# Kernel tuning notes

Hardware: AMD Instinct MI355X
Metric: run time of the kernel (lower is better)

## Reference

```python
import jax, jax.numpy as jnp
import numpy as np

B, LQ, S, D, H = 8, 1024, 256, 1024, 16
HD = D // H
LN_EPS = 1e-5


def layer_norm(x, g, b):
    m = jnp.mean(x, axis=-1, keepdims=True)
    v = jnp.mean((x - m) ** 2, axis=-1, keepdims=True)
    return (x - m) / jnp.sqrt(v + LN_EPS) * g + b


def setup_inputs() -> dict:
    key = jax.random.key(0)
    ks = jax.random.split(key, 12)
    sc = 0.02
    p = lambda k, shp: jax.random.normal(k, shp, dtype=jnp.float32) * sc
    return {
        "memory": jax.random.normal(ks[0], (B, LQ, D // 2), dtype=jnp.float32),
        "gaze_features": jax.random.normal(ks[1], (B, LQ, D // 2), dtype=jnp.float32),
        "text_features": jax.random.normal(ks[2], (B, S, D), dtype=jnp.float32),
        "w_in": p(ks[3], (3 * D, D)),  # packed q,k,v in_proj (torch MHA layout)
        "b_in": jnp.zeros((3 * D,), jnp.float32),
        "w_o": p(ks[4], (D, D)),
        "b_o": jnp.zeros((D,), jnp.float32),
        "w1": p(ks[5], (D, D)),
        "b1": jnp.zeros((D,), jnp.float32),
        "w2": p(ks[6], (D, D)),
        "b2": jnp.zeros((D,), jnp.float32),
        "g1": jnp.ones((D,), jnp.float32),
        "be1": jnp.zeros((D,), jnp.float32),
        "g2": jnp.ones((D,), jnp.float32),
        "be2": jnp.zeros((D,), jnp.float32),
    }


def reference(memory, gaze_features, text_features, w_in, b_in, w_o, b_o,
              w1, b1, w2, b2, g1, be1, g2, be2):
    combined = jnp.concatenate([memory, gaze_features], axis=-1)  # [B, LQ, D]
    wq, wk, wv = w_in[:D], w_in[D:2 * D], w_in[2 * D:]
    bq, bk, bv = b_in[:D], b_in[D:2 * D], b_in[2 * D:]

    q = (combined @ wq.T + bq).reshape(B, LQ, H, HD)
    k = (text_features @ wk.T + bk).reshape(B, S, H, HD)
    v = (text_features @ wv.T + bv).reshape(B, S, H, HD)

    scores = jnp.einsum("bqhd,bkhd->bhqk", q, k) / jnp.sqrt(jnp.float32(HD))
    attn_w = jax.nn.softmax(scores, axis=-1)
    ctx = jnp.einsum("bhqk,bkhd->bqhd", attn_w, v).reshape(B, LQ, D)
    attn_output = ctx @ w_o.T + b_o  # [B, LQ, D]

    # dual FFN branches share linear1/linear2 (as in the source); dropout = eval identity
    ffn = jax.nn.relu(attn_output @ w1.T + b1) @ w2.T + b2
    refpoint_embed = layer_norm(ffn, g1, be1)
    tgt = layer_norm(ffn, g2, be2)

    # vectorized box decode (replaces the per-element Python loop)
    s = jax.nn.sigmoid(attn_output[..., :4])
    xc, yc, w, h = s[..., 0], s[..., 1], s[..., 2], s[..., 3]
    init_box_proposal = jnp.stack(
        [xc - w / 2, yc - h / 2, xc + w / 2, yc + h / 2], axis=-1)  # [B, LQ, 4]

    return refpoint_embed, tgt, init_box_proposal
```

## Files before the change

### kernel.cpp

```cpp
#include <hip/hip_runtime.h>


typedef unsigned short u16;
typedef unsigned int u32;
typedef __bf16 bf16x8 __attribute__((ext_vector_type(8)));
typedef float f32x4 __attribute__((ext_vector_type(4)));
typedef u16 u16x4 __attribute__((ext_vector_type(4)));

struct CvtArgs { const void* in[15]; };

__device__ __forceinline__ u16 f2bf(float f) {
  u32 u = __builtin_bit_cast(u32, f);
  u += 0x7fffu + ((u >> 16) & 1u);
  return (u16)(u >> 16);
}
__device__ __forceinline__ float bf2f(u16 h) {
  u32 u = ((u32)h) << 16;
  return __builtin_bit_cast(float, u);
}

struct WsPtrs {
  u16 *c_mem, *c_gaze, *c_text, *c_win, *c_bin, *c_wo, *c_bo, *c_w1, *c_b1,
      *c_w2, *c_b2, *c_g1, *c_be1, *c_g2, *c_be2;
  u16 *q, *k, *v, *ctx, *woT, *wf, *bfb, *h1;
  float* ffn;
};
__device__ __forceinline__ WsPtrs wsp(u16* C) {
  WsPtrs w;
  w.c_mem = C;                 w.c_gaze = C + 4194304;   w.c_text = C + 8388608;
  w.c_win = C + 10485760;      w.c_bin = C + 13631488;   w.c_wo = C + 13634560;
  w.c_bo = C + 14683136;       w.c_w1 = C + 14684160;    w.c_b1 = C + 15732736;
  w.c_w2 = C + 15733760;       w.c_b2 = C + 16782336;    w.c_g1 = C + 16783360;
  w.c_be1 = C + 16784384;      w.c_g2 = C + 16785408;    w.c_be2 = C + 16786432;
  u16* B2 = C + 16787488;
  w.q = B2;                    w.k = B2 + 8388608;       w.v = B2 + 10485760;
  w.ctx = B2 + 12582912;
  w.woT = B2 + 20971520;
  w.wf  = B2 + 22020096;
  w.bfb = B2 + 23068672;
  w.h1  = B2 + 29360128;
  w.ffn = (float*)B2;
  return w;
}

__device__ __forceinline__ void cvt_chunk(bool f32in, u16* dst,
                                          const void* const* srcs, u32 c8) {
  const u32 cum[16] = {0u, 4194304u, 8388608u, 10485760u, 13631488u, 13634560u,
                       14683136u, 14684160u, 15732736u, 15733760u, 16782336u,
                       16783360u, 16784384u, 16785408u, 16786432u, 16787456u};
  u32 base = c8 * 8u;
  int idx = 0;
#pragma unroll
  for (int i = 1; i < 15; ++i) if (base >= cum[i]) idx = i;
  u32 off = base - cum[idx];
  if (f32in) {
    const float* s = (const float*)srcs[idx] + off;
    float4 a = ((const float4*)s)[0];
    float4 b = ((const float4*)s)[1];
    u16 t[8] = {f2bf(a.x), f2bf(a.y), f2bf(a.z), f2bf(a.w),
                f2bf(b.x), f2bf(b.y), f2bf(b.z), f2bf(b.w)};
    *(uint4*)(dst + base) = *(const uint4*)t;
  } else {
    *(uint4*)(dst + base) = *(const uint4*)((const u16*)srcs[idx] + off);
  }
}

__global__ __launch_bounds__(256) void cvt_tr(CvtArgs a, u16* ws) {
  __shared__ u16 tile[128 * 136];
  const bool f32in = (((const u32*)a.in[11])[0] == 0x3F800000u);
  const int bid = blockIdx.x, tid = threadIdx.x;
  if (bid < 64) {
    WsPtrs w = wsp(ws);
    int tr = bid >> 3, tc = bid & 7;
#pragma unroll
    for (int p = 0; p < 8; ++p) {
      int t = p * 16 + (tid >> 4);
      int j8 = (tid & 15) * 8;
      u16 tmp[8];
      if (f32in) {
        const float* s = (const float*)a.in[5] + (size_t)(tr * 128 + t) * 1024 + tc * 128 + j8;
        float4 x = ((const float4*)s)[0], y = ((const float4*)s)[1];
        tmp[0]=f2bf(x.x); tmp[1]=f2bf(x.y); tmp[2]=f2bf(x.z); tmp[3]=f2bf(x.w);
        tmp[4]=f2bf(y.x); tmp[5]=f2bf(y.y); tmp[6]=f2bf(y.z); tmp[7]=f2bf(y.w);
      } else {
        *(uint4*)tmp = *(const uint4*)((const u16*)a.in[5] + (size_t)(tr * 128 + t) * 1024 + tc * 128 + j8);
      }
      *(uint4*)&tile[t * 136 + j8] = *(const uint4*)tmp;
    }
    __syncthreads();
#pragma unroll
    for (int p = 0; p < 8; ++p) {
      int j = p * 16 + (tid >> 4);
      int t8 = (tid & 15) * 8;
      u16 tmp[8];
#pragma unroll
      for (int i = 0; i < 8; ++i) tmp[i] = tile[(t8 + i) * 136 + j];
      *(uint4*)(w.woT + (size_t)(tc * 128 + j) * 1024 + tr * 128 + t8) = *(const uint4*)tmp;
    }
  } else {
    u32 c8 = (u32)(bid - 64) * 256u + tid;
    if (c8 < 2098432u) cvt_chunk(f32in, ws, a.in, c8);
  }
}

__device__ __forceinline__ void gemm_core(
    u16* sA, u16* sB,
    const u16* A0, const u16* A1, int Ksplit, int lda0, int lda1,
    const u16* W, const u16* bias, void* out, int N, int K,
    int mode, int lg, int m0, int n0)
{
  const int tid = threadIdx.x;
  const int wave = tid >> 6, lane = tid & 63;
  const int quad = lane >> 4, l16 = lane & 15;
  const int wm = wave >> 1, wn = wave & 1;

  f32x4 acc[4][4];
#pragma unroll
  for (int i = 0; i < 4; ++i)
#pragma unroll
    for (int j = 0; j < 4; ++j) acc[i][j] = (f32x4){0.f, 0.f, 0.f, 0.f};

  for (int k0 = 0; k0 < K; k0 += 128) {
#pragma unroll
    for (int qi = 0; qi < 8; ++qi) {
      int p = (wave * 8 + qi) * 64 + lane;
      int row = p >> 4;
      int c = (p & 15) ^ (row & 7);
      int gk = k0 + (c << 3);
      const u16* srcA = (gk < Ksplit) ? (A0 + (size_t)(m0 + row) * lda0 + gk)
                                      : (A1 + (size_t)(m0 + row) * lda1 + (gk - Ksplit));
      __builtin_amdgcn_global_load_lds(
          (const __attribute__((address_space(1))) void*)srcA,
          (__attribute__((address_space(3))) void*)&sA[(size_t)(wave * 8 + qi) * 512],
          16, 0, 0);
      const u16* srcB = W + (size_t)(n0 + row) * K + gk;
      __builtin_amdgcn_global_load_lds(
          (const __attribute__((address_space(1))) void*)srcB,
          (__attribute__((address_space(3))) void*)&sB[(size_t)(wave * 8 + qi) * 512],
          16, 0, 0);
    }
    __syncthreads();
#pragma unroll
    for (int ks = 0; ks < 4; ++ks) {
      const int ch = (ks << 2) + quad;
      bf16x8 af[4], bw[4];
#pragma unroll
      for (int i = 0; i < 4; ++i) {
        int row = wm * 64 + i * 16 + l16;
        af[i] = *(const bf16x8*)&sA[(row << 7) + ((ch ^ (row & 7)) << 3)];
      }
#pragma unroll
      for (int j = 0; j < 4; ++j) {
        int row = wn * 64 + j * 16 + l16;
        bw[j] = *(const bf16x8*)&sB[(row << 7) + ((ch ^ (row & 7)) << 3)];
      }
#pragma unroll
      for (int i = 0; i < 4; ++i)
#pragma unroll
        for (int j = 0; j < 4; ++j)
          acc[i][j] = __builtin_amdgcn_mfma_f32_16x16x32_bf16(af[i], bw[j], acc[i][j], 0, 0, 0);
    }
    __syncthreads();
  }

#pragma unroll
  for (int i = 0; i < 4; ++i) {
#pragma unroll
    for (int j = 0; j < 4; ++j) {
      int n = n0 + wn * 64 + j * 16 + l16;
      float bv = bias ? bf2f(bias[n]) : 0.f;
#pragma unroll
      for (int rr = 0; rr < 4; ++rr) {
        int m = m0 + wm * 64 + i * 16 + quad * 4 + rr;
        float val = acc[i][j][rr] + bv;
        if (mode == 1) val = fmaxf(val, 0.f);
        if (mode == 2) {
          ((float*)out)[(size_t)m * N + n] = val;
        } else if (mode <= 1) {
          ((u16*)out)[(size_t)m * N + n] = f2bf(val);
        } else if (mode == 3) {
          int b = m >> lg, l = m & ((1 << lg) - 1);
          int h = n >> 6, d = n & 63;
          ((u16*)out)[((size_t)((b * 16 + h)) << (lg + 6)) + (l << 6) + d] = f2bf(val);
        } else {
          int b = m >> lg, s = m & ((1 << lg) - 1);
          int h = n >> 6, d = n & 63;
          ((u16*)out)[((size_t)(((b * 16 + h) << 6) + d) << lg) + s] = f2bf(val);
        }
      }
    }
  }
}

__global__ __launch_bounds__(256) void qkvwf(u16* ws) {
  __shared__ u16 lds[32768];
  WsPtrs w = wsp(ws);
  const int bid = blockIdx.x, tid = threadIdx.x;
  if (bid < 4) {
    int i = bid * 256 + tid;
    const u16* w1row = w.c_w1 + (size_t)i * 1024;
    float acc = bf2f(w.c_b1[i]);
    for (int kk = 0; kk < 1024; kk += 8) {
      bf16x8 wv = *(const bf16x8*)(w1row + kk);
      bf16x8 bv = *(const bf16x8*)(w.c_bo + kk);
#pragma unroll
      for (int j = 0; j < 8; ++j) acc += (float)wv[j] * (float)bv[j];
    }
    w.bfb[i] = f2bf(acc);
  } else if (bid < 68) {
    int u = bid - 4;
    gemm_core(lds, lds + 16384, w.c_w1, w.c_w1, 1024, 1024, 1024,
              w.woT, nullptr, w.wf, 1024, 1024, 0, 0,
              (u >> 3) * 128, (u & 7) * 128);
  } else if (bid < 580) {
    int u = bid - 68;
    gemm_core(lds, lds + 16384, w.c_mem, w.c_gaze, 512, 512, 512,
              w.c_win, w.c_bin, w.q, 1024, 1024, 3, 10,
              (u >> 3) * 128, (u & 7) * 128);
  } else if (bid < 708) {
    int u = bid - 580;
    gemm_core(lds, lds + 16384, w.c_text, w.c_text, 1024, 1024, 1024,
              w.c_win + 1048576, w.c_bin + 1024, w.k, 1024, 1024, 3, 8,
              (u >> 3) * 128, (u & 7) * 128);
  } else {
    int u = bid - 708;
    gemm_core(lds, lds + 16384, w.c_text, w.c_text, 1024, 1024, 1024,
              w.c_win + 2097152, w.c_bin + 2048, w.v, 1024, 1024, 4, 8,
              (u >> 3) * 128, (u & 7) * 128);
  }
}

__global__ __launch_bounds__(256) void attn_kernel(u16* ws) {
  __shared__ u16 sV[64 * 256];
  __shared__ u16 sKP[256 * 64];
  WsPtrs w = wsp(ws);
  const int tid = threadIdx.x;
  const int wave = tid >> 6, lane = tid & 63;
  const int quad = lane >> 4, l16 = lane & 15;
  const int qb = blockIdx.x & 15, bh = blockIdx.x >> 4;

  {
    int rr = tid >> 3, c8 = (tid & 7) << 3;
    const u16* kb = w.k + (size_t)bh * 16384;
#pragma unroll
    for (int p = 0; p < 8; ++p) {
      int row = p * 32 + rr;
      uint4 val = *(const uint4*)(kb + row * 64 + c8);
      *(uint4*)&sKP[(row << 6) + ((((c8 >> 3) ^ (row & 7))) << 3)] = val;
    }
    int r2 = tid >> 5, c8b = (tid & 31) << 3;
    const u16* vb = w.v + (size_t)bh * 16384;
#pragma unroll
    for (int p = 0; p < 8; ++p) {
      int row = p * 8 + r2;
      uint4 val = *(const uint4*)(vb + (row << 8) + c8b);
      *(uint4*)&sV[(row << 8) + ((((c8b >> 3) ^ (row & 7))) << 3)] = val;
    }
  }
  bf16x8 aq[2];
  {
    const u16* qrow = w.q + ((size_t)bh * 1024 + qb * 64 + wave * 16 + l16) * 64 + quad * 8;
    aq[0] = *(const bf16x8*)(qrow);
    aq[1] = *(const bf16x8*)(qrow + 32);
  }
  __syncthreads();

  f32x4 sc[16];
#pragma unroll
  for (int nt = 0; nt < 16; ++nt) sc[nt] = (f32x4){0.f, 0.f, 0.f, 0.f};
#pragma unroll
  for (int ks = 0; ks < 2; ++ks) {
    const int ch = (ks << 2) + quad;
#pragma unroll
    for (int nt = 0; nt < 16; ++nt) {
      int row = nt * 16 + l16;
      bf16x8 bk = *(const bf16x8*)&sKP[(row << 6) + ((ch ^ (row & 7)) << 3)];
      sc[nt] = __builtin_amdgcn_mfma_f32_16x16x32_bf16(aq[ks], bk, sc[nt], 0, 0, 0);
    }
  }
#pragma unroll
  for (int rr = 0; rr < 4; ++rr) {
    float mx = -1e30f;
#pragma unroll
    for (int nt = 0; nt < 16; ++nt) mx = fmaxf(mx, sc[nt][rr]);
    for (int off = 1; off < 16; off <<= 1) mx = fmaxf(mx, __shfl_xor(mx, off, 64));
    float sum = 0.f;
#pragma unroll
    for (int nt = 0; nt < 16; ++nt) {
      float p = __expf((sc[nt][rr] - mx) * 0.125f);
      sc[nt][rr] = p; sum += p;
    }
    for (int off = 1; off < 16; off <<= 1) sum += __shfl_xor(sum, off, 64);
    float inv = 1.f / sum;
#pragma unroll
    for (int nt = 0; nt < 16; ++nt) sc[nt][rr] *= inv;
  }
  __syncthreads();
#pragma unroll
  for (int nt = 0; nt < 16; ++nt)
#pragma unroll
    for (int rr = 0; rr < 4; ++rr) {
      int row = wave * 16 + quad * 4 + rr;
      int col = nt * 16 + l16;
      sKP[(row << 8) + (((col >> 3) ^ (row & 7)) << 3) + (col & 7)] = f2bf(sc[nt][rr]);
    }
  __syncthreads();

  f32x4 o[4];
#pragma unroll
  for (int j = 0; j < 4; ++j) o[j] = (f32x4){0.f, 0.f, 0.f, 0.f};
#pragma unroll
  for (int ks = 0; ks < 8; ++ks) {
    const int ch = (ks << 2) + quad;
    int prow = wave * 16 + l16;
    bf16x8 ap = *(const bf16x8*)&sKP[(prow << 8) + ((ch ^ (prow & 7)) << 3)];
#pragma unroll
    for (int j = 0; j < 4; ++j) {
      int vrow = j * 16 + l16;
      bf16x8 bv = *(const bf16x8*)&sV[(vrow << 8) + ((ch ^ (vrow & 7)) << 3)];
      o[j] = __builtin_amdgcn_mfma_f32_16x16x32_bf16(ap, bv, o[j], 0, 0, 0);
    }
  }
  const int b = bh >> 4, h = bh & 15;
#pragma unroll
  for (int j = 0; j < 4; ++j)
#pragma unroll
    for (int rr = 0; rr < 4; ++rr) {
      int m = qb * 64 + wave * 16 + quad * 4 + rr;
      int d = h * 64 + j * 16 + l16;
      w.ctx[((size_t)b * 1024 + m) * 1024 + d] = f2bf(o[j][rr]);
    }
}

__global__ __launch_bounds__(256) void h1box(u16* ws, void* out, const void* g1orig) {
  __shared__ u16 lds[32768];
  WsPtrs w = wsp(ws);
  const int bid = blockIdx.x, tid = threadIdx.x;
  if (bid < 32) {
    const bool f32out = (((const u32*)g1orig)[0] == 0x3F800000u);
    int m = bid * 256 + tid;
    const u16* crow = w.ctx + (size_t)m * 1024;
    float a0 = bf2f(w.c_bo[0]), a1 = bf2f(w.c_bo[1]);
    float a2 = bf2f(w.c_bo[2]), a3 = bf2f(w.c_bo[3]);
    for (int kk = 0; kk < 1024; kk += 8) {
      bf16x8 cv = *(const bf16x8*)(crow + kk);
      bf16x8 w0 = *(const bf16x8*)(w.c_wo + kk);
      bf16x8 w1 = *(const bf16x8*)(w.c_wo + 1024 + kk);
      bf16x8 w2 = *(const bf16x8*)(w.c_wo + 2048 + kk);
      bf16x8 w3 = *(const bf16x8*)(w.c_wo + 3072 + kk);
#pragma unroll
      for (int j = 0; j < 8; ++j) {
        float c = (float)cv[j];
        a0 += c * (float)w0[j]; a1 += c * (float)w1[j];
        a2 += c * (float)w2[j]; a3 += c * (float)w3[j];
      }
    }
    float s0 = 1.f / (1.f + __expf(-a0)), s1 = 1.f / (1.f + __expf(-a1));
    float s2 = 1.f / (1.f + __expf(-a2)), s3 = 1.f / (1.f + __expf(-a3));
    float o0 = s0 - s2 * 0.5f, o1 = s1 - s3 * 0.5f;
    float o2 = s0 + s2 * 0.5f, o3 = s1 + s3 * 0.5f;
    if (f32out) {
      float* fo = (float*)out + 16777216;
      *(float4*)(fo + (size_t)m * 4) = make_float4(o0, o1, o2, o3);
    } else {
      u16* bo = (u16*)out + 16777216;
      u16x4 o; o[0] = f2bf(o0); o[1] = f2bf(o1); o[2] = f2bf(o2); o[3] = f2bf(o3);
      *(u16x4*)(bo + (size_t)m * 4) = o;
    }
  } else {
    int u = bid - 32;
    gemm_core(lds, lds + 16384, w.ctx, w.ctx, 1024, 1024, 1024,
              w.wf, w.bfb, w.h1, 1024, 1024, 1, 0,
              (u >> 3) * 128, (u & 7) * 128);
  }
}

__global__ __launch_bounds__(256) void w2gemm(u16* ws) {
  __shared__ u16 lds[32768];
  WsPtrs w = wsp(ws);
  gemm_core(lds, lds + 16384, w.h1, w.h1, 1024, 1024, 1024,
            w.c_w2, w.c_b2, w.ffn, 1024, 1024, 2, 0,
            (blockIdx.x >> 3) * 128, (blockIdx.x & 7) * 128);
}

__global__ __launch_bounds__(256) void ln_kernel(u16* ws, void* outv, const void* g1orig) {
  WsPtrs w = wsp(ws);
  const bool f32out = (((const u32*)g1orig)[0] == 0x3F800000u);
  const int row = blockIdx.x, tid = threadIdx.x;
  const float4 x4 = ((const float4*)(w.ffn + (size_t)row * 1024))[tid];
  float s = x4.x + x4.y + x4.z + x4.w;
  float s2 = x4.x * x4.x + x4.y * x4.y + x4.z * x4.z + x4.w * x4.w;
  for (int m = 32; m >= 1; m >>= 1) { s += __shfl_xor(s, m, 64); s2 += __shfl_xor(s2, m, 64); }
  __shared__ float red[8];
  int wv = tid >> 6;
  if ((tid & 63) == 0) { red[wv] = s; red[4 + wv] = s2; }
  __syncthreads();
  s = red[0] + red[1] + red[2] + red[3];
  s2 = red[4] + red[5] + red[6] + red[7];
  float mean = s * (1.f / 1024.f);
  float var = s2 * (1.f / 1024.f) - mean * mean;
  float inv = rsqrtf(var + 1e-5f);
  int c = tid * 4;
  float y[4] = {(x4.x - mean) * inv, (x4.y - mean) * inv, (x4.z - mean) * inv, (x4.w - mean) * inv};
  float v1[4], v2[4];
#pragma unroll
  for (int i = 0; i < 4; ++i) {
    v1[i] = y[i] * bf2f(w.c_g1[c + i]) + bf2f(w.c_be1[c + i]);
    v2[i] = y[i] * bf2f(w.c_g2[c + i]) + bf2f(w.c_be2[c + i]);
  }
  if (f32out) {
    float* fo = (float*)outv;
    *(float4*)(fo + (size_t)row * 1024 + c) = make_float4(v1[0], v1[1], v1[2], v1[3]);
    *(float4*)(fo + 8388608 + (size_t)row * 1024 + c) = make_float4(v2[0], v2[1], v2[2], v2[3]);
  } else {
    u16* out = (u16*)outv;
    u16x4 o1, o2;
#pragma unroll
    for (int i = 0; i < 4; ++i) { o1[i] = f2bf(v1[i]); o2[i] = f2bf(v2[i]); }
    *(u16x4*)(out + (size_t)row * 1024 + c) = o1;
    *(u16x4*)(out + 8388608 + (size_t)row * 1024 + c) = o2;
  }
}

extern "C" void kernel_launch(void* const* d_in, const int* in_sizes, int n_in,
                              void* d_out, int out_size, void* d_ws, size_t ws_size,
                              hipStream_t stream) {
  CvtArgs ca;
  for (int i = 0; i < 15; ++i) ca.in[i] = d_in[i];
  u16* ws = (u16*)d_ws;
  dim3 blk(256);
  cvt_tr<<<dim3(8261), blk, 0, stream>>>(ca, ws);
  qkvwf<<<dim3(836), blk, 0, stream>>>(ws);
  attn_kernel<<<dim3(2048), blk, 0, stream>>>(ws);
  h1box<<<dim3(544), blk, 0, stream>>>(ws, d_out, d_in[11]);
  w2gemm<<<dim3(512), blk, 0, stream>>>(ws);
  ln_kernel<<<dim3(8192), blk, 0, stream>>>(ws, d_out, d_in[11]);
}
```

Baseline: 313.6 us.

## Fuse box decode, FFN GEMMs and layernorm into one persistent kernel with atomic counters

Merges the box/h1 kernel, the W2 GEMM and the layernorm kernel into a single 512-block kernel. Cross-block dependencies are handled with global atomic row-tile counters and ticket-based work assignment, and the counters are reset at the start of the attention kernel. The FFN intermediate is now stored in bf16 instead of fp32, and the box decode is split across 16 lanes per row. It also reorders the blocks in qkvwf so the big Q GEMM is scheduled first. The goal is to remove launch gaps and the fp32 round trip, at the cost of spin-wait synchronisation that depends on all blocks being co-resident, plus reduced precision for the LN input.

```diff
diff --git a/kernel.cpp b/kernel.cpp
--- a/kernel.cpp
+++ b/kernel.cpp
@@ -18,12 +18,19 @@
   u32 u = ((u32)h) << 16;
   return __builtin_bit_cast(float, u);
 }
-
+__device__ __forceinline__ u32 aadd(u32* p) {
+  return __hip_atomic_fetch_add(p, 1u, __ATOMIC_RELAXED, __HIP_MEMORY_SCOPE_AGENT);
+}
+__device__ __forceinline__ u32 aload(const u32* p) {
+  return __hip_atomic_load(p, __ATOMIC_RELAXED, __HIP_MEMORY_SCOPE_AGENT);
+}
+
+#define B2OFF 16787488
+#define SYNC_U32 ((B2OFF + 23069696) / 2)
 struct WsPtrs {
   u16 *c_mem, *c_gaze, *c_text, *c_win, *c_bin, *c_wo, *c_bo, *c_w1, *c_b1,
       *c_w2, *c_b2, *c_g1, *c_be1, *c_g2, *c_be2;
-  u16 *q, *k, *v, *ctx, *woT, *wf, *bfb, *h1;
-  float* ffn;
+  u16 *q, *k, *v, *ctx, *woT, *wf, *bfb, *h1, *ffnb;
 };
 __device__ __forceinline__ WsPtrs wsp(u16* C) {
   WsPtrs w;
@@ -32,14 +39,14 @@
   w.c_bo = C + 14683136;       w.c_w1 = C + 14684160;    w.c_b1 = C + 15732736;
   w.c_w2 = C + 15733760;       w.c_b2 = C + 16782336;    w.c_g1 = C + 16783360;
   w.c_be1 = C + 16784384;      w.c_g2 = C + 16785408;    w.c_be2 = C + 16786432;
-  u16* B2 = C + 16787488;
+  u16* B2 = C + B2OFF;
   w.q = B2;                    w.k = B2 + 8388608;       w.v = B2 + 10485760;
   w.ctx = B2 + 12582912;
   w.woT = B2 + 20971520;
   w.wf  = B2 + 22020096;
   w.bfb = B2 + 23068672;
   w.h1  = B2 + 29360128;
-  w.ffn = (float*)B2;
+  w.ffnb = B2;
   return w;
 }
 
@@ -174,9 +181,7 @@
         int m = m0 + wm * 64 + i * 16 + quad * 4 + rr;
         float val = acc[i][j][rr] + bv;
         if (mode == 1) val = fmaxf(val, 0.f);
-        if (mode == 2) {
-          ((float*)out)[(size_t)m * N + n] = val;
-        } else if (mode <= 1) {
+        if (mode <= 1) {
           ((u16*)out)[(size_t)m * N + n] = f2bf(val);
         } else if (mode == 3) {
           int b = m >> lg, l = m & ((1 << lg) - 1);
@@ -196,8 +201,27 @@
   __shared__ u16 lds[32768];
   WsPtrs w = wsp(ws);
   const int bid = blockIdx.x, tid = threadIdx.x;
-  if (bid < 4) {
-    int i = bid * 256 + tid;
+  if (bid < 512) {
+    gemm_core(lds, lds + 16384, w.c_mem, w.c_gaze, 512, 512, 512,
+              w.c_win, w.c_bin, w.q, 1024, 1024, 3, 10,
+              (bid >> 3) * 128, (bid & 7) * 128);
+  } else if (bid < 640) {
+    int u = bid - 512;
+    gemm_core(lds, lds + 16384, w.c_text, w.c_text, 1024, 1024, 1024,
+              w.c_win + 1048576, w.c_bin + 1024, w.k, 1024, 1024, 3, 8,
+              (u >> 3) * 128, (u & 7) * 128);
+  } else if (bid < 768) {
+    int u = bid - 640;
+    gemm_core(lds, lds + 16384, w.c_text, w.c_text, 1024, 1024, 1024,
+              w.c_win + 2097152, w.c_bin + 2048, w.v, 1024, 1024, 4, 8,
+              (u >> 3) * 128, (u & 7) * 128);
+  } else if (bid < 832) {
+    int u = bid - 768;
+    gemm_core(lds, lds + 16384, w.c_w1, w.c_w1, 1024, 1024, 1024,
+              w.woT, nullptr, w.wf, 1024, 1024, 0, 0,
+              (u >> 3) * 128, (u & 7) * 128);
+  } else {
+    int i = (bid - 832) * 256 + tid;
     const u16* w1row = w.c_w1 + (size_t)i * 1024;
     float acc = bf2f(w.c_b1[i]);
     for (int kk = 0; kk < 1024; kk += 8) {
@@ -207,26 +231,6 @@
       for (int j = 0; j < 8; ++j) acc += (float)wv[j] * (float)bv[j];
     }
     w.bfb[i] = f2bf(acc);
-  } else if (bid < 68) {
-    int u = bid - 4;
-    gemm_core(lds, lds + 16384, w.c_w1, w.c_w1, 1024, 1024, 1024,
-              w.woT, nullptr, w.wf, 1024, 1024, 0, 0,
-              (u >> 3) * 128, (u & 7) * 128);
-  } else if (bid < 580) {
-    int u = bid - 68;
-    gemm_core(lds, lds + 16384, w.c_mem, w.c_gaze, 512, 512, 512,
-              w.c_win, w.c_bin, w.q, 1024, 1024, 3, 10,
-              (u >> 3) * 128, (u & 7) * 128);
-  } else if (bid < 708) {
-    int u = bid - 580;
-    gemm_core(lds, lds + 16384, w.c_text, w.c_text, 1024, 1024, 1024,
-              w.c_win + 1048576, w.c_bin + 1024, w.k, 1024, 1024, 3, 8,
-              (u >> 3) * 128, (u & 7) * 128);
-  } else {
-    int u = bid - 708;
-    gemm_core(lds, lds + 16384, w.c_text, w.c_text, 1024, 1024, 1024,
-              w.c_win + 2097152, w.c_bin + 2048, w.v, 1024, 1024, 4, 8,
-              (u >> 3) * 128, (u & 7) * 128);
   }
 }
 
@@ -235,6 +239,7 @@
   __shared__ u16 sKP[256 * 64];
   WsPtrs w = wsp(ws);
   const int tid = threadIdx.x;
+  if (blockIdx.x == 0 && tid < 130) ((u32*)ws)[SYNC_U32 + tid] = 0;
   const int wave = tid >> 6, lane = tid & 63;
   const int quad = lane >> 4, l16 = lane & 15;
   const int qb = blockIdx.x & 15, bh = blockIdx.x >> 4;
@@ -332,22 +337,30 @@
     }
 }
 
-__global__ __launch_bounds__(256) void h1box(u16* ws, void* out, const void* g1orig) {
+__global__ __launch_bounds__(256, 2) void ffn_mega(u16* ws, void* out, const void* g1orig) {
   __shared__ u16 lds[32768];
+  __shared__ u32 s_t;
   WsPtrs w = wsp(ws);
-  const int bid = blockIdx.x, tid = threadIdx.x;
-  if (bid < 32) {
-    const bool f32out = (((const u32*)g1orig)[0] == 0x3F800000u);
-    int m = bid * 256 + tid;
-    const u16* crow = w.ctx + (size_t)m * 1024;
-    float a0 = bf2f(w.c_bo[0]), a1 = bf2f(w.c_bo[1]);
-    float a2 = bf2f(w.c_bo[2]), a3 = bf2f(w.c_bo[3]);
-    for (int kk = 0; kk < 1024; kk += 8) {
+  u32* cnt1 = (u32*)ws + SYNC_U32;
+  u32* cnt2 = cnt1 + 64;
+  u32* tick1 = cnt1 + 128;
+  u32* tick2 = cnt1 + 129;
+  const bool f32out = (((const u32*)g1orig)[0] == 0x3F800000u);
+  const int u = blockIdx.x, tid = threadIdx.x;
+  const int r16 = tid >> 4, l4 = tid & 15;
+
+  {
+    int m = u * 16 + r16;
+    int k0 = l4 * 64;
+    const u16* crow = w.ctx + (size_t)m * 1024 + k0;
+    float a0 = 0.f, a1 = 0.f, a2 = 0.f, a3 = 0.f;
+#pragma unroll
+    for (int kk = 0; kk < 64; kk += 8) {
       bf16x8 cv = *(const bf16x8*)(crow + kk);
-      bf16x8 w0 = *(const bf16x8*)(w.c_wo + kk);
-      bf16x8 w1 = *(const bf16x8*)(w.c_wo + 1024 + kk);
-      bf16x8 w2 = *(const bf16x8*)(w.c_wo + 2048 + kk);
-      bf16x8 w3 = *(const bf16x8*)(w.c_wo + 3072 + kk);
+      bf16x8 w0 = *(const bf16x8*)(w.c_wo + k0 + kk);
+      bf16x8 w1 = *(const bf16x8*)(w.c_wo + 1024 + k0 + kk);
+      bf16x8 w2 = *(const bf16x8*)(w.c_wo + 2048 + k0 + kk);
+      bf16x8 w3 = *(const bf16x8*)(w.c_wo + 3072 + k0 + kk);
 #pragma unroll
       for (int j = 0; j < 8; ++j) {
         float c = (float)cv[j];
@@ -355,70 +368,116 @@
         a2 += c * (float)w2[j]; a3 += c * (float)w3[j];
       }
     }
-    float s0 = 1.f / (1.f + __expf(-a0)), s1 = 1.f / (1.f + __expf(-a1));
-    float s2 = 1.f / (1.f + __expf(-a2)), s3 = 1.f / (1.f + __expf(-a3));
-    float o0 = s0 - s2 * 0.5f, o1 = s1 - s3 * 0.5f;
-    float o2 = s0 + s2 * 0.5f, o3 = s1 + s3 * 0.5f;
-    if (f32out) {
-      float* fo = (float*)out + 16777216;
-      *(float4*)(fo + (size_t)m * 4) = make_float4(o0, o1, o2, o3);
-    } else {
-      u16* bo = (u16*)out + 16777216;
-      u16x4 o; o[0] = f2bf(o0); o[1] = f2bf(o1); o[2] = f2bf(o2); o[3] = f2bf(o3);
-      *(u16x4*)(bo + (size_t)m * 4) = o;
-    }
-  } else {
-    int u = bid - 32;
-    gemm_core(lds, lds + 16384, w.ctx, w.ctx, 1024, 1024, 1024,
-              w.wf, w.bfb, w.h1, 1024, 1024, 1, 0,
-              (u >> 3) * 128, (u & 7) * 128);
-  }
-}
-
-__global__ __launch_bounds__(256) void w2gemm(u16* ws) {
-  __shared__ u16 lds[32768];
-  WsPtrs w = wsp(ws);
-  gemm_core(lds, lds + 16384, w.h1, w.h1, 1024, 1024, 1024,
-            w.c_w2, w.c_b2, w.ffn, 1024, 1024, 2, 0,
-            (blockIdx.x >> 3) * 128, (blockIdx.x & 7) * 128);
-}
-
-__global__ __launch_bounds__(256) void ln_kernel(u16* ws, void* outv, const void* g1orig) {
-  WsPtrs w = wsp(ws);
-  const bool f32out = (((const u32*)g1orig)[0] == 0x3F800000u);
-  const int row = blockIdx.x, tid = threadIdx.x;
-  const float4 x4 = ((const float4*)(w.ffn + (size_t)row * 1024))[tid];
-  float s = x4.x + x4.y + x4.z + x4.w;
-  float s2 = x4.x * x4.x + x4.y * x4.y + x4.z * x4.z + x4.w * x4.w;
-  for (int m = 32; m >= 1; m >>= 1) { s += __shfl_xor(s, m, 64); s2 += __shfl_xor(s2, m, 64); }
-  __shared__ float red[8];
-  int wv = tid >> 6;
-  if ((tid & 63) == 0) { red[wv] = s; red[4 + wv] = s2; }
-  __syncthreads();
-  s = red[0] + red[1] + red[2] + red[3];
-  s2 = red[4] + red[5] + red[6] + red[7];
-  float mean = s * (1.f / 1024.f);
-  float var = s2 * (1.f / 1024.f) - mean * mean;
-  float inv = rsqrtf(var + 1e-5f);
-  int c = tid * 4;
-  float y[4] = {(x4.x - mean) * inv, (x4.y - mean) * inv, (x4.z - mean) * inv, (x4.w - mean) * inv};
-  float v1[4], v2[4];
-#pragma unroll
-  for (int i = 0; i < 4; ++i) {
-    v1[i] = y[i] * bf2f(w.c_g1[c + i]) + bf2f(w.c_be1[c + i]);
-    v2[i] = y[i] * bf2f(w.c_g2[c + i]) + bf2f(w.c_be2[c + i]);
-  }
-  if (f32out) {
-    float* fo = (float*)outv;
-    *(float4*)(fo + (size_t)row * 1024 + c) = make_float4(v1[0], v1[1], v1[2], v1[3]);
-    *(float4*)(fo + 8388608 + (size_t)row * 1024 + c) = make_float4(v2[0], v2[1], v2[2], v2[3]);
-  } else {
-    u16* out = (u16*)outv;
-    u16x4 o1, o2;
-#pragma unroll
-    for (int i = 0; i < 4; ++i) { o1[i] = f2bf(v1[i]); o2[i] = f2bf(v2[i]); }
-    *(u16x4*)(out + (size_t)row * 1024 + c) = o1;
-    *(u16x4*)(out + 8388608 + (size_t)row * 1024 + c) = o2;
+    for (int off = 1; off < 16; off <<= 1) {
+      a0 += __shfl_xor(a0, off, 64); a1 += __shfl_xor(a1, off, 64);
+      a2 += __shfl_xor(a2, off, 64); a3 += __shfl_xor(a3, off, 64);
+    }
+    if (l4 == 0) {
+      a0 += bf2f(w.c_bo[0]); a1 += bf2f(w.c_bo[1]);
+      a2 += bf2f(w.c_bo[2]); a3 += bf2f(w.c_bo[3]);
+      float s0 = 1.f / (1.f + __expf(-a0)), s1 = 1.f / (1.f + __expf(-a1));
+      float s2 = 1.f / (1.f + __expf(-a2)), s3 = 1.f / (1.f + __expf(-a3));
+      float o0 = s0 - s2 * 0.5f, o1 = s1 - s3 * 0.5f;
+      float o2 = s0 + s2 * 0.5f, o3 = s1 + s3 * 0.5f;
+      if (f32out) {
+        float* fo = (float*)out + 16777216;
+        *(float4*)(fo + (size_t)m * 4) = make_float4(o0, o1, o2, o3);
+      } else {
+        u16* bo = (u16*)out + 16777216;
+        u16x4 o; o[0] = f2bf(o0); o[1] = f2bf(o1); o[2] = f2bf(o2); o[3] = f2bf(o3);
+        *(u16x4*)(bo + (size_t)m * 4) = o;
+      }
+    }
+  }
+
+  gemm_core(lds, lds + 16384, w.ctx, w.ctx, 1024, 1024, 1024,
+            w.wf, w.bfb, w.h1, 1024, 1024, 1, 0, (u >> 3) * 128, (u & 7) * 128);
+  __syncthreads();
+  if (tid == 0) { __threadfence(); aadd(&cnt1[u >> 3]); }
+
+  if (tid == 0) s_t = aadd(tick1);
+  __syncthreads();
+  {
+    u32 t = s_t;
+    int ms2 = t >> 3;
+    if (tid == 0) {
+      while (aload(&cnt1[ms2]) < 8u) __builtin_amdgcn_s_sleep(16);
+      __threadfence();
+    }
+    __syncthreads();
+    gemm_core(lds, lds + 16384, w.h1, w.h1, 1024, 1024, 1024,
+              w.c_w2, w.c_b2, w.ffnb, 1024, 1024, 0, 0, ms2 * 128, (t & 7) * 128);
+    __syncthreads();
+    if (tid == 0) { __threadfence(); aadd(&cnt2[ms2]); }
+  }
+
+  if (tid == 0) s_t = aadd(tick2);
+  __syncthreads();
+  {
+    u32 t2 = s_t;
+    if (t2 < 64u) {
+      if (tid == 0) {
+        while (aload(&cnt2[t2]) < 8u) __builtin_amdgcn_s_sleep(16);
+        __threadfence();
+      }
+      __syncthreads();
+#pragma unroll
+      for (int rr = 0; rr < 8; ++rr) {
+        int row = (int)t2 * 128 + rr * 16 + r16;
+        int c0 = l4 * 64;
+        const u16* fr = w.ffnb + (size_t)row * 1024 + c0;
+        float s = 0.f, s2 = 0.f;
+#pragma unroll
+        for (int kk = 0; kk < 64; kk += 8) {
+          bf16x8 xv = *(const bf16x8*)(fr + kk);
+#pragma unroll
+          for (int j = 0; j < 8; ++j) { float x = (float)xv[j]; s += x; s2 += x * x; }
+        }
+        for (int off = 1; off < 16; off <<= 1) {
+          s += __shfl_xor(s, off, 64); s2 += __shfl_xor(s2, off, 64);
+        }
+        float mean = s * (1.f / 1024.f);
+        float var = s2 * (1.f / 1024.f) - mean * mean;
+        float inv = rsqrtf(var + 1e-5f);
+        if (f32out) {
+          float* fo = (float*)out;
+#pragma unroll
+          for (int kk = 0; kk < 64; kk += 8) {
+            bf16x8 xv = *(const bf16x8*)(fr + kk);
+            float t1v[8], t2v[8];
+#pragma unroll
+            for (int j = 0; j < 8; ++j) {
+              float y = ((float)xv[j] - mean) * inv;
+              int c = c0 + kk + j;
+              t1v[j] = y * bf2f(w.c_g1[c]) + bf2f(w.c_be1[c]);
+              t2v[j] = y * bf2f(w.c_g2[c]) + bf2f(w.c_be2[c]);
+            }
+            size_t o1 = (size_t)row * 1024 + c0 + kk;
+            *(float4*)(fo + o1) = make_float4(t1v[0], t1v[1], t1v[2], t1v[3]);
+            *(float4*)(fo + o1 + 4) = make_float4(t1v[4], t1v[5], t1v[6], t1v[7]);
+            *(float4*)(fo + 8388608 + o1) = make_float4(t2v[0], t2v[1], t2v[2], t2v[3]);
+            *(float4*)(fo + 8388608 + o1 + 4) = make_float4(t2v[4], t2v[5], t2v[6], t2v[7]);
+          }
+        } else {
+          u16* uo = (u16*)out;
+#pragma unroll
+          for (int kk = 0; kk < 64; kk += 8) {
+            bf16x8 xv = *(const bf16x8*)(fr + kk);
+            u16 t1v[8], t2v[8];
+#pragma unroll
+            for (int j = 0; j < 8; ++j) {
+              float y = ((float)xv[j] - mean) * inv;
+              int c = c0 + kk + j;
+              t1v[j] = f2bf(y * bf2f(w.c_g1[c]) + bf2f(w.c_be1[c]));
+              t2v[j] = f2bf(y * bf2f(w.c_g2[c]) + bf2f(w.c_be2[c]));
+            }
+            size_t o1 = (size_t)row * 1024 + c0 + kk;
+            *(uint4*)(uo + o1) = *(const uint4*)t1v;
+            *(uint4*)(uo + 8388608 + o1) = *(const uint4*)t2v;
+          }
+        }
+      }
+    }
   }
 }
 
@@ -432,7 +491,5 @@
   cvt_tr<<<dim3(8261), blk, 0, stream>>>(ca, ws);
   qkvwf<<<dim3(836), blk, 0, stream>>>(ws);
   attn_kernel<<<dim3(2048), blk, 0, stream>>>(ws);
-  h1box<<<dim3(544), blk, 0, stream>>>(ws, d_out, d_in[11]);
-  w2gemm<<<dim3(512), blk, 0, stream>>>(ws);
-  ln_kernel<<<dim3(8192), blk, 0, stream>>>(ws, d_out, d_in[11]);
-}
+  ffn_mega<<<dim3(512), blk, 0, stream>>>(ws, d_out, d_in[11]);
+}
```

Measured after the change: 527.6 us. 1.68x slower.

## Store FFN output in bf16, spread box decode across GEMM blocks, reorder qkvwf blocks

Applied to the files above, without the earlier changes.

The FFN output written by the second GEMM is stored as bf16 instead of fp32, which halves the traffic between that GEMM and the layer-norm kernel. The box-decode dot products used to run in 32 serial tail blocks. They are now split across all 512 h1 GEMM blocks, with 16 lanes per row and a shuffle reduction before each block does its GEMM tile. The qkvwf block ordering is also changed so the large Q/K/V GEMM tiles are scheduled first and the small bias dot-product blocks come last. The cost is lower precision on the FFN intermediate before layer norm.

```diff
diff --git a/kernel.cpp b/kernel.cpp
--- a/kernel.cpp
+++ b/kernel.cpp
@@ -22,8 +22,7 @@
 struct WsPtrs {
   u16 *c_mem, *c_gaze, *c_text, *c_win, *c_bin, *c_wo, *c_bo, *c_w1, *c_b1,
       *c_w2, *c_b2, *c_g1, *c_be1, *c_g2, *c_be2;
-  u16 *q, *k, *v, *ctx, *woT, *wf, *bfb, *h1;
-  float* ffn;
+  u16 *q, *k, *v, *ctx, *woT, *wf, *bfb, *h1, *ffnb;
 };
 __device__ __forceinline__ WsPtrs wsp(u16* C) {
   WsPtrs w;
@@ -39,7 +38,7 @@
   w.wf  = B2 + 22020096;
   w.bfb = B2 + 23068672;
   w.h1  = B2 + 29360128;
-  w.ffn = (float*)B2;
+  w.ffnb = B2;
   return w;
 }
 
@@ -174,9 +173,7 @@
         int m = m0 + wm * 64 + i * 16 + quad * 4 + rr;
         float val = acc[i][j][rr] + bv;
         if (mode == 1) val = fmaxf(val, 0.f);
-        if (mode == 2) {
-          ((float*)out)[(size_t)m * N + n] = val;
-        } else if (mode <= 1) {
+        if (mode <= 1) {
           ((u16*)out)[(size_t)m * N + n] = f2bf(val);
         } else if (mode == 3) {
           int b = m >> lg, l = m & ((1 << lg) - 1);
@@ -196,8 +193,27 @@
   __shared__ u16 lds[32768];
   WsPtrs w = wsp(ws);
   const int bid = blockIdx.x, tid = threadIdx.x;
-  if (bid < 4) {
-    int i = bid * 256 + tid;
+  if (bid < 512) {
+    gemm_core(lds, lds + 16384, w.c_mem, w.c_gaze, 512, 512, 512,
+              w.c_win, w.c_bin, w.q, 1024, 1024, 3, 10,
+              (bid >> 3) * 128, (bid & 7) * 128);
+  } else if (bid < 640) {
+    int u = bid - 512;
+    gemm_core(lds, lds + 16384, w.c_text, w.c_text, 1024, 1024, 1024,
+              w.c_win + 1048576, w.c_bin + 1024, w.k, 1024, 1024, 3, 8,
+              (u >> 3) * 128, (u & 7) * 128);
+  } else if (bid < 768) {
+    int u = bid - 640;
+    gemm_core(lds, lds + 16384, w.c_text, w.c_text, 1024, 1024, 1024,
+              w.c_win + 2097152, w.c_bin + 2048, w.v, 1024, 1024, 4, 8,
+              (u >> 3) * 128, (u & 7) * 128);
+  } else if (bid < 832) {
+    int u = bid - 768;
+    gemm_core(lds, lds + 16384, w.c_w1, w.c_w1, 1024, 1024, 1024,
+              w.woT, nullptr, w.wf, 1024, 1024, 0, 0,
+              (u >> 3) * 128, (u & 7) * 128);
+  } else {
+    int i = (bid - 832) * 256 + tid;
     const u16* w1row = w.c_w1 + (size_t)i * 1024;
     float acc = bf2f(w.c_b1[i]);
     for (int kk = 0; kk < 1024; kk += 8) {
@@ -207,26 +223,6 @@
       for (int j = 0; j < 8; ++j) acc += (float)wv[j] * (float)bv[j];
     }
     w.bfb[i] = f2bf(acc);
-  } else if (bid < 68) {
-    int u = bid - 4;
-    gemm_core(lds, lds + 16384, w.c_w1, w.c_w1, 1024, 1024, 1024,
-              w.woT, nullptr, w.wf, 1024, 1024, 0, 0,
-              (u >> 3) * 128, (u & 7) * 128);
-  } else if (bid < 580) {
-    int u = bid - 68;
-    gemm_core(lds, lds + 16384, w.c_mem, w.c_gaze, 512, 512, 512,
-              w.c_win, w.c_bin, w.q, 1024, 1024, 3, 10,
-              (u >> 3) * 128, (u & 7) * 128);
-  } else if (bid < 708) {
-    int u = bid - 580;
-    gemm_core(lds, lds + 16384, w.c_text, w.c_text, 1024, 1024, 1024,
-              w.c_win + 1048576, w.c_bin + 1024, w.k, 1024, 1024, 3, 8,
-              (u >> 3) * 128, (u & 7) * 128);
-  } else {
-    int u = bid - 708;
-    gemm_core(lds, lds + 16384, w.c_text, w.c_text, 1024, 1024, 1024,
-              w.c_win + 2097152, w.c_bin + 2048, w.v, 1024, 1024, 4, 8,
-              (u >> 3) * 128, (u & 7) * 128);
   }
 }
 
@@ -335,19 +331,21 @@
 __global__ __launch_bounds__(256) void h1box(u16* ws, void* out, const void* g1orig) {
   __shared__ u16 lds[32768];
   WsPtrs w = wsp(ws);
-  const int bid = blockIdx.x, tid = threadIdx.x;
-  if (bid < 32) {
+  const int u = blockIdx.x, tid = threadIdx.x;
+  const int r16 = tid >> 4, l4 = tid & 15;
+  {
     const bool f32out = (((const u32*)g1orig)[0] == 0x3F800000u);
-    int m = bid * 256 + tid;
-    const u16* crow = w.ctx + (size_t)m * 1024;
-    float a0 = bf2f(w.c_bo[0]), a1 = bf2f(w.c_bo[1]);
-    float a2 = bf2f(w.c_bo[2]), a3 = bf2f(w.c_bo[3]);
-    for (int kk = 0; kk < 1024; kk += 8) {
+    int m = u * 16 + r16;
+    int k0 = l4 * 64;
+    const u16* crow = w.ctx + (size_t)m * 1024 + k0;
+    float a0 = 0.f, a1 = 0.f, a2 = 0.f, a3 = 0.f;
+#pragma unroll
+    for (int kk = 0; kk < 64; kk += 8) {
       bf16x8 cv = *(const bf16x8*)(crow + kk);
-      bf16x8 w0 = *(const bf16x8*)(w.c_wo + kk);
-      bf16x8 w1 = *(const bf16x8*)(w.c_wo + 1024 + kk);
-      bf16x8 w2 = *(const bf16x8*)(w.c_wo + 2048 + kk);
-      bf16x8 w3 = *(const bf16x8*)(w.c_wo + 3072 + kk);
+      bf16x8 w0 = *(const bf16x8*)(w.c_wo + k0 + kk);
+      bf16x8 w1 = *(const bf16x8*)(w.c_wo + 1024 + k0 + kk);
+      bf16x8 w2 = *(const bf16x8*)(w.c_wo + 2048 + k0 + kk);
+      bf16x8 w3 = *(const bf16x8*)(w.c_wo + 3072 + k0 + kk);
 #pragma unroll
       for (int j = 0; j < 8; ++j) {
         float c = (float)cv[j];
@@ -355,31 +353,36 @@
         a2 += c * (float)w2[j]; a3 += c * (float)w3[j];
       }
     }
-    float s0 = 1.f / (1.f + __expf(-a0)), s1 = 1.f / (1.f + __expf(-a1));
-    float s2 = 1.f / (1.f + __expf(-a2)), s3 = 1.f / (1.f + __expf(-a3));
-    float o0 = s0 - s2 * 0.5f, o1 = s1 - s3 * 0.5f;
-    float o2 = s0 + s2 * 0.5f, o3 = s1 + s3 * 0.5f;
-    if (f32out) {
-      float* fo = (float*)out + 16777216;
-      *(float4*)(fo + (size_t)m * 4) = make_float4(o0, o1, o2, o3);
-    } else {
-      u16* bo = (u16*)out + 16777216;
-      u16x4 o; o[0] = f2bf(o0); o[1] = f2bf(o1); o[2] = f2bf(o2); o[3] = f2bf(o3);
-      *(u16x4*)(bo + (size_t)m * 4) = o;
-    }
-  } else {
-    int u = bid - 32;
-    gemm_core(lds, lds + 16384, w.ctx, w.ctx, 1024, 1024, 1024,
-              w.wf, w.bfb, w.h1, 1024, 1024, 1, 0,
-              (u >> 3) * 128, (u & 7) * 128);
-  }
+    for (int off = 1; off < 16; off <<= 1) {
+      a0 += __shfl_xor(a0, off, 64); a1 += __shfl_xor(a1, off, 64);
+      a2 += __shfl_xor(a2, off, 64); a3 += __shfl_xor(a3, off, 64);
+    }
+    if (l4 == 0) {
+      a0 += bf2f(w.c_bo[0]); a1 += bf2f(w.c_bo[1]);
+      a2 += bf2f(w.c_bo[2]); a3 += bf2f(w.c_bo[3]);
+      float s0 = 1.f / (1.f + __expf(-a0)), s1 = 1.f / (1.f + __expf(-a1));
+      float s2 = 1.f / (1.f + __expf(-a2)), s3 = 1.f / (1.f + __expf(-a3));
+      float o0 = s0 - s2 * 0.5f, o1 = s1 - s3 * 0.5f;
+      float o2 = s0 + s2 * 0.5f, o3 = s1 + s3 * 0.5f;
+      if (f32out) {
+        float* fo = (float*)out + 16777216;
+        *(float4*)(fo + (size_t)m * 4) = make_float4(o0, o1, o2, o3);
+      } else {
+        u16* bo = (u16*)out + 16777216;
+        u16x4 o; o[0] = f2bf(o0); o[1] = f2bf(o1); o[2] = f2bf(o2); o[3] = f2bf(o3);
+        *(u16x4*)(bo + (size_t)m * 4) = o;
+      }
+    }
+  }
+  gemm_core(lds, lds + 16384, w.ctx, w.ctx, 1024, 1024, 1024,
+            w.wf, w.bfb, w.h1, 1024, 1024, 1, 0, (u >> 3) * 128, (u & 7) * 128);
 }
 
 __global__ __launch_bounds__(256) void w2gemm(u16* ws) {
   __shared__ u16 lds[32768];
   WsPtrs w = wsp(ws);
   gemm_core(lds, lds + 16384, w.h1, w.h1, 1024, 1024, 1024,
-            w.c_w2, w.c_b2, w.ffn, 1024, 1024, 2, 0,
+            w.c_w2, w.c_b2, w.ffnb, 1024, 1024, 0, 0,
             (blockIdx.x >> 3) * 128, (blockIdx.x & 7) * 128);
 }
 
@@ -387,9 +390,11 @@
   WsPtrs w = wsp(ws);
   const bool f32out = (((const u32*)g1orig)[0] == 0x3F800000u);
   const int row = blockIdx.x, tid = threadIdx.x;
-  const float4 x4 = ((const float4*)(w.ffn + (size_t)row * 1024))[tid];
-  float s = x4.x + x4.y + x4.z + x4.w;
-  float s2 = x4.x * x4.x + x4.y * x4.y + x4.z * x4.z + x4.w * x4.w;
+  int c = tid * 4;
+  u16x4 xr = *(const u16x4*)(w.ffnb + (size_t)row * 1024 + c);
+  float x[4] = {bf2f(xr[0]), bf2f(xr[1]), bf2f(xr[2]), bf2f(xr[3])};
+  float s = x[0] + x[1] + x[2] + x[3];
+  float s2 = x[0]*x[0] + x[1]*x[1] + x[2]*x[2] + x[3]*x[3];
   for (int m = 32; m >= 1; m >>= 1) { s += __shfl_xor(s, m, 64); s2 += __shfl_xor(s2, m, 64); }
   __shared__ float red[8];
   int wv = tid >> 6;
@@ -400,8 +405,7 @@
   float mean = s * (1.f / 1024.f);
   float var = s2 * (1.f / 1024.f) - mean * mean;
   float inv = rsqrtf(var + 1e-5f);
-  int c = tid * 4;
-  float y[4] = {(x4.x - mean) * inv, (x4.y - mean) * inv, (x4.z - mean) * inv, (x4.w - mean) * inv};
+  float y[4] = {(x[0] - mean) * inv, (x[1] - mean) * inv, (x[2] - mean) * inv, (x[3] - mean) * inv};
   float v1[4], v2[4];
 #pragma unroll
   for (int i = 0; i < 4; ++i) {
@@ -432,7 +436,7 @@
   cvt_tr<<<dim3(8261), blk, 0, stream>>>(ca, ws);
   qkvwf<<<dim3(836), blk, 0, stream>>>(ws);
   attn_kernel<<<dim3(2048), blk, 0, stream>>>(ws);
-  h1box<<<dim3(544), blk, 0, stream>>>(ws, d_out, d_in[11]);
+  h1box<<<dim3(512), blk, 0, stream>>>(ws, d_out, d_in[11]);
   w2gemm<<<dim3(512), blk, 0, stream>>>(ws);
   ln_kernel<<<dim3(8192), blk, 0, stream>>>(ws, d_out, d_in[11]);
 }
```

Result: faster. 301.3 us (-3.9%).
